# Kernel tuning notes

Hardware: AMD Instinct MI355X
Metric: run time of the kernel (lower is better)

## Reference

```python
import jax, jax.numpy as jnp
import numpy as np

DIM = 2048
NH = 16
NKV = 4
HD = DIM // NH            # 128
KVD = HD * NKV            # 512
MLP = int(DIM * 4.0 * 2 / 3)  # 5461
EPS = 1.1920929e-07       # torch.finfo(float32).eps (nn.RMSNorm default)
ROPE_BASE = 10000.0


def act_quant(x):
    # per-token int8 absmax quantization (BitNet b1.58)
    scale = 127.0 / jnp.clip(jnp.max(jnp.abs(x), axis=-1, keepdims=True), 1e-5)
    return jnp.clip(jnp.round(x * scale), -128.0, 127.0) / scale


def weight_quant(w):
    # ternary weights via mean-absmax scale (BitNet b1.58)
    scale = 1.0 / jnp.clip(jnp.mean(jnp.abs(w)), 1e-5)
    return jnp.clip(jnp.round(w * scale), -1.0, 1.0) / scale


def bitlinear(x, w, b=None):
    # straight-through estimator quantization, then dense matmul
    xq = x + jax.lax.stop_gradient(act_quant(x) - x)
    wq = w + jax.lax.stop_gradient(weight_quant(w) - w)
    y = xq @ wq.T
    return y if b is None else y + b


def rmsnorm(x, w):
    return x * jax.lax.rsqrt(jnp.mean(x * x, axis=-1, keepdims=True) + EPS) * w


def rope_cos_sin(pos, head_dim, dtype):
    inv_freq = 1.0 / (ROPE_BASE ** (jnp.arange(0, head_dim, 2, dtype=jnp.float32) / head_dim))
    freqs = pos[..., None].astype(jnp.float32) * inv_freq  # [B,N,HD/2]
    cos = jnp.repeat(jnp.cos(freqs), 2, axis=-1).astype(dtype)  # interleaved [B,N,HD]
    sin = jnp.repeat(jnp.sin(freqs), 2, axis=-1).astype(dtype)
    return cos, sin


def rotate_interleave(x):
    x1 = x[..., 0::2]
    x2 = x[..., 1::2]
    return jnp.stack([-x2, x1], axis=-1).reshape(x.shape)


def apply_rope(x, cos, sin):
    # x: [B,H,N,HD]; cos/sin: [B,N,HD]
    return x * cos[:, None] + rotate_interleave(x) * sin[:, None]


def setup_inputs() -> dict:
    key = jax.random.key(0)
    ks = jax.random.split(key, 16)
    B, N = 2, 2048
    s = 0.02
    return {
        "x": jax.random.normal(ks[0], (B, N, DIM), jnp.float32),
        "position_ids": jnp.broadcast_to(jnp.arange(N, dtype=jnp.int32), (B, N)),
        "norm1_w": jnp.ones((DIM,), jnp.float32),
        "q_w": jax.random.normal(ks[1], (DIM, DIM), jnp.float32) * s,
        "q_b": jnp.zeros((DIM,), jnp.float32),
        "k_w": jax.random.normal(ks[2], (KVD, DIM), jnp.float32) * s,
        "k_b": jnp.zeros((KVD,), jnp.float32),
        "v_w": jax.random.normal(ks[3], (KVD, DIM), jnp.float32) * s,
        "v_b": jnp.zeros((KVD,), jnp.float32),
        "o_w": jax.random.normal(ks[4], (DIM, DIM), jnp.float32) * s,
        "norm2_w": jnp.ones((DIM,), jnp.float32),
        "gate_w": jax.random.normal(ks[5], (MLP, DIM), jnp.float32) * s,
        "up_w": jax.random.normal(ks[6], (MLP, DIM), jnp.float32) * s,
        "down_w": jax.random.normal(ks[7], (DIM, MLP), jnp.float32) * s,
    }


def reference(x, position_ids, norm1_w, q_w, q_b, k_w, k_b, v_w, v_b, o_w,
              norm2_w, gate_w, up_w, down_w):
    B, N, C = x.shape
    # --- attention ---
    h = rmsnorm(x, norm1_w)
    q = bitlinear(h, q_w, q_b).reshape(B, N, NH, HD).transpose(0, 2, 1, 3)
    k = bitlinear(h, k_w, k_b).reshape(B, N, NKV, HD).transpose(0, 2, 1, 3)
    v = bitlinear(h, v_w, v_b).reshape(B, N, NKV, HD).transpose(0, 2, 1, 3)
    cos, sin = rope_cos_sin(position_ids, HD, x.dtype)
    q = apply_rope(q, cos, sin)
    k = apply_rope(k, cos, sin)
    g = NH // NKV
    k = jnp.repeat(k, g, axis=1)  # GQA head expansion -> [B,NH,N,HD]
    v = jnp.repeat(v, g, axis=1)
    scores = jnp.einsum('bhqd,bhkd->bhqk', q, k) * (HD ** -0.5)
    causal_mask = jnp.triu(jnp.ones((N, N), bool), 1)
    scores = jnp.where(causal_mask, -jnp.inf, scores)
    attn = jax.nn.softmax(scores, axis=-1)
    out = jnp.einsum('bhqk,bhkd->bqhd', attn, v).reshape(B, N, C)
    x = x + bitlinear(out, o_w)
    # --- SwiGLU MLP ---
    h = rmsnorm(x, norm2_w)
    x = x + bitlinear(jax.nn.silu(bitlinear(h, gate_w)) * bitlinear(h, up_w), down_w)
    return x
```

## Files before the change

kernel.cpp:

```cpp
#include <hip/hip_runtime.h>

typedef unsigned short u16;
typedef unsigned int   u32;
typedef unsigned char  u8;

using bf16x8 = __attribute__((ext_vector_type(8))) short;
using f32x4  = __attribute__((ext_vector_type(4))) float;
using i32x4  = __attribute__((ext_vector_type(4))) int;

#define SEQ    2048
#define DIMC   2048
#define TOK    4096
#define QKV_N  3072
#define GU_N   11008
#define MLP_P  5504
#define MLP_R  5461
#define ATT_SCALE 0.08838834764831845f

__device__ __forceinline__ float bf2f(u16 v){ return __uint_as_float(((u32)v) << 16); }
__device__ __forceinline__ u16 f2bf(float f){
  u32 x = __float_as_uint(f);
  u32 r = (x + 0x7fffu + ((x >> 16) & 1u)) >> 16;
  return (u16)r;
}

__device__ __forceinline__ float waveRedSum(float v){
#pragma unroll
  for (int o = 32; o > 0; o >>= 1) v += __shfl_xor(v, o);
  return v;
}
__device__ __forceinline__ float waveRedMax(float v){
#pragma unroll
  for (int o = 32; o > 0; o >>= 1) v = fmaxf(v, __shfl_xor(v, o));
  return v;
}

#define GLD16(gp, lp) __builtin_amdgcn_global_load_lds( \
    (__attribute__((address_space(1))) void*)(gp), \
    (__attribute__((address_space(3))) void*)(lp), 16, 0, 0)

#define FENCE() asm volatile("" ::: "memory")
#define SBAR()  do{ FENCE(); __builtin_amdgcn_s_barrier(); FENCE(); }while(0)
#define VMCNT(n) asm volatile("s_waitcnt vmcnt(" #n ")" ::: "memory")

__global__ __launch_bounds__(256) void k_abssum7(
    const float4* __restrict__ w0, const float4* __restrict__ w1,
    const float4* __restrict__ w2, const float4* __restrict__ w3,
    const float4* __restrict__ w4, const float4* __restrict__ w5,
    const float4* __restrict__ w6, float* __restrict__ sc){
  const int rg = blockIdx.y;
  const float4* w = rg==0?w0: rg==1?w1: rg==2?w2: rg==3?w3: rg==4?w4: rg==5?w5: w6;
  const int n4 = (rg==0||rg==3) ? 1048576 : (rg<4 ? 262144 : 2796032);
  float s = 0.f;
  for (int i = blockIdx.x*256 + threadIdx.x; i < n4; i += gridDim.x*256){
    float4 v = w[i];
    s += fabsf(v.x) + fabsf(v.y) + fabsf(v.z) + fabsf(v.w);
  }
  s = waveRedSum(s);
  __shared__ float sm[4];
  int lane = threadIdx.x & 63, wv = threadIdx.x >> 6;
  if (lane == 0) sm[wv] = s;
  __syncthreads();
  if (threadIdx.x == 0) atomicAdd(sc + rg, sm[0]+sm[1]+sm[2]+sm[3]);
}

__global__ void k_finalize(float* __restrict__ sc){
  if (threadIdx.x == 0){
    const float counts[7] = {4194304.f, 1048576.f, 1048576.f, 4194304.f,
                             11184128.f, 11184128.f, 11184128.f};
    for (int i = 0; i < 7; i++) sc[8+i] = fmaxf(sc[i]/counts[i], 1e-5f);
  }
}

__global__ __launch_bounds__(256) void k_wquant6(
    const float4* __restrict__ w0, const float4* __restrict__ w1,
    const float4* __restrict__ w2, const float4* __restrict__ w3,
    const float4* __restrict__ w4, const float4* __restrict__ w5,
    u32* __restrict__ d0, u32* __restrict__ d1, u32* __restrict__ d2,
    u32* __restrict__ d3, u32* __restrict__ dgu,
    const float* __restrict__ sc){
  const int rg = blockIdx.y;
  const float4* src = rg==0?w0: rg==1?w1: rg==2?w2: rg==3?w3: rg==4?w4: w5;
  const int n4 = (rg==0||rg==3) ? 1048576 : (rg<4 ? 262144 : 2796032);
  float ws = 1.0f / sc[8+rg];
  for (int i = blockIdx.x*256 + threadIdx.x; i < n4; i += gridDim.x*256){
    float4 v = src[i];
    int c0 = (int)fminf(fmaxf(rintf(v.x*ws), -1.f), 1.f);
    int c1 = (int)fminf(fmaxf(rintf(v.y*ws), -1.f), 1.f);
    int c2 = (int)fminf(fmaxf(rintf(v.z*ws), -1.f), 1.f);
    int c3 = (int)fminf(fmaxf(rintf(v.w*ws), -1.f), 1.f);
    u32 pk = (u32)(u8)c0 | ((u32)(u8)c1 << 8) | ((u32)(u8)c2 << 16) | ((u32)(u8)c3 << 24);
    if (rg < 4){
      u32* dst = rg==0?d0: rg==1?d1: rg==2?d2: d3;
      dst[i] = pk;
    } else {
      int row = i >> 9, col = i & 511;
      int rI = 32*(row>>4) + (row&15) + ((rg==5)?16:0);
      dgu[(long)rI*512 + col] = pk;
    }
  }
}

__global__ __launch_bounds__(256) void k_wquant_down(const float* __restrict__ src,
                                                     u32* __restrict__ dst,
                                                     const float* __restrict__ deqp){
  int i = blockIdx.x*256 + threadIdx.x;
  const int total = 2048*(MLP_P/4);
  if (i >= total) return;
  float ws = 1.0f / deqp[0];
  int r = i / (MLP_P/4);
  int c4 = (i - r*(MLP_P/4))*4;
  u32 o = 0;
#pragma unroll
  for (int e = 0; e < 4; e++){
    int c = c4 + e;
    int t = 0;
    if (c < MLP_R) t = (int)fminf(fmaxf(rintf(src[(long)r*MLP_R + c]*ws), -1.f), 1.f);
    o |= (u32)(u8)t << (8*e);
  }
  dst[i] = o;
}

__global__ __launch_bounds__(256) void k_rmsq(const float* __restrict__ in,
                                              const float* __restrict__ nw,
                                              char* __restrict__ outq,
                                              float* __restrict__ rowdeq, int do_norm){
  const int row = blockIdx.x, tid = threadIdx.x;
  const float* xp = in + (long)row * DIMC + tid*8;
  float v[8];
  float4 a0 = *(const float4*)xp;
  float4 a1 = *(const float4*)(xp + 4);
  v[0]=a0.x; v[1]=a0.y; v[2]=a0.z; v[3]=a0.w;
  v[4]=a1.x; v[5]=a1.y; v[6]=a1.z; v[7]=a1.w;
  float ss = 0.f;
#pragma unroll
  for (int j = 0; j < 8; j++) ss += v[j]*v[j];
  __shared__ float sm[8];
  int lane = tid & 63, wv = tid >> 6;
  ss = waveRedSum(ss);
  if (lane == 0) sm[wv] = ss;
  __syncthreads();
  float h[8];
  float amax = 0.f;
  if (do_norm){
    float tot = sm[0]+sm[1]+sm[2]+sm[3];
    float rms = rsqrtf(tot * (1.0f/DIMC) + 1.1920929e-07f);
    float4 w0 = *(const float4*)(nw + tid*8);
    float4 w1 = *(const float4*)(nw + tid*8 + 4);
    float wr8[8] = {w0.x,w0.y,w0.z,w0.w,w1.x,w1.y,w1.z,w1.w};
#pragma unroll
    for (int j = 0; j < 8; j++){ h[j] = v[j]*rms*wr8[j]; amax = fmaxf(amax, fabsf(h[j])); }
  } else {
#pragma unroll
    for (int j = 0; j < 8; j++){ h[j] = v[j]; amax = fmaxf(amax, fabsf(h[j])); }
  }
  amax = waveRedMax(amax);
  if (lane == 0) sm[4+wv] = amax;
  __syncthreads();
  float gmax = fmaxf(fmaxf(sm[4],sm[5]), fmaxf(sm[6],sm[7]));
  float sc = 127.0f / fmaxf(gmax, 1e-5f);
  int2 o;
  char* oc = (char*)&o;
#pragma unroll
  for (int j = 0; j < 8; j++)
    oc[j] = (char)(int)fminf(fmaxf(rintf(h[j]*sc), -128.f), 127.f);
  *(int2*)(outq + (long)row*DIMC + tid*8) = o;
  if (tid == 0) rowdeq[row] = 1.0f / sc;
}

__global__ __launch_bounds__(256) void k_quantb(const u16* __restrict__ in,
                                                char* __restrict__ outq,
                                                float* __restrict__ rowdeq){
  const int row = blockIdx.x, tid = threadIdx.x;
  int4 a = *(const int4*)(in + (long)row*DIMC + tid*8);
  const u16* ap = (const u16*)&a;
  float v[8];
  float amax = 0.f;
#pragma unroll
  for (int j = 0; j < 8; j++){ v[j] = bf2f(ap[j]); amax = fmaxf(amax, fabsf(v[j])); }
  amax = waveRedMax(amax);
  __shared__ float sm[4];
  int lane = tid & 63, wv = tid >> 6;
  if (lane == 0) sm[wv] = amax;
  __syncthreads();
  float gmax = fmaxf(fmaxf(sm[0],sm[1]), fmaxf(sm[2],sm[3]));
  float sc = 127.0f / fmaxf(gmax, 1e-5f);
  int2 o;
  char* oc = (char*)&o;
#pragma unroll
  for (int j = 0; j < 8; j++)
    oc[j] = (char)(int)fminf(fmaxf(rintf(v[j]*sc), -128.f), 127.f);
  *(int2*)(outq + (long)row*DIMC + tid*8) = o;
  if (tid == 0) rowdeq[row] = 1.0f / sc;
}

__global__ __launch_bounds__(256) void k_ropevt2(u16* __restrict__ y,
                                                 const int* __restrict__ pos_ids,
                                                 u16* __restrict__ VT){
  if (blockIdx.x < 4096){
    const int m = blockIdx.x, tid = threadIdx.x;
    __shared__ float cs[64], sn[64];
    if (tid < 64){
      float pos = (float)pos_ids[m];
      float inv = expf((float)tid * -0.14391156831212787f);
      float s, c;
      sincosf(pos * inv, &s, &c);
      cs[tid] = c; sn[tid] = s;
    }
    __syncthreads();
    u32* row = (u32*)(y + (long)m*QKV_N);
#pragma unroll
    for (int it = 0; it < 5; it++){
      int p = it*256 + tid;
      int i = p & 63;
      u32 both = row[p];
      float x0 = bf2f((u16)(both & 0xffffu));
      float x1 = bf2f((u16)(both >> 16));
      float c = cs[i], s = sn[i];
      u16 o0 = f2bf(x0*c - x1*s);
      u16 o1 = f2bf(x1*c + x0*s);
      row[p] = (u32)o0 | ((u32)o1 << 16);
    }
  } else {
    int idx = (int)(blockIdx.x - 4096)*256 + threadIdx.x;
    int d  = idx & 127;
    int hk = (idx >> 7) & 3;
    int b  = (idx >> 9) & 1;
    int tg = idx >> 10;
    int tok0 = tg*8;
    const u16* src = y + ((long)b*SEQ + tok0)*QKV_N + 2560 + hk*128 + d;
    u16 tmp[8];
#pragma unroll
    for (int e = 0; e < 8; e++) tmp[e] = src[(long)e*QKV_N];
    *(int4*)(VT + (((long)(b*4+hk))*128 + d)*SEQ + tok0) = *(int4*)tmp;
  }
}

template<int BM, int BN, int WM, int WN, int MODE>
__global__ __launch_bounds__(512, 2) void k_gemm8(
    const char* __restrict__ A, const char* __restrict__ B,
    int K, int lda, int ldb, int ldc, int ntn,
    const float* __restrict__ rowdeq, const float* __restrict__ deqp,
    const float* __restrict__ bq, const float* __restrict__ bk, const float* __restrict__ bv,
    const float* __restrict__ resid, float* __restrict__ outF, u16* __restrict__ outB)
{
  constexpr int SM = BM/WM, SN = BN/WN;
  constexpr int MR = SM/16, NR = SN/16, MRH = MR/2;
  constexpr int RA = BM/128, RB = BN/128;
  constexpr int ASZ = BM*64, BSZ = BN*64;
  constexpr int BUFSZ = 2*(ASZ+BSZ);
  extern __shared__ __align__(16) char sm8[];

  const int tid = threadIdx.x;
  const int lane = tid & 63, wv = tid >> 6;
  const int wr = wv / WN, wc = wv % WN;
  const int r = lane & 15, qq = lane >> 4;

  const int nwg = gridDim.x;
  const int chunk = nwg >> 3;
  const int lin = blockIdx.x;
  const int swz = (lin & 7)*chunk + (lin >> 3);
  const int mt = swz / ntn, nt = swz - mt*ntn;
  const long m0 = (long)mt*BM, n0 = (long)nt*BN;

  const char* __restrict__ gA = A + m0*lda;
  const char* __restrict__ gB = B + n0*ldb;

  int  soA[RA], soB[RB];
  long goA[RA], goB[RB];
#pragma unroll
  for (int u = 0; u < RA; u++){
    int c = u*512 + tid, row = c >> 2, gp = c & 3, g = gp ^ ((row>>1)&3);
    soA[u] = c*16; goA[u] = (long)row*lda + g*16;
  }
#pragma unroll
  for (int u = 0; u < RB; u++){
    int c = u*512 + tid, row = c >> 2, gp = c & 3, g = gp ^ ((row>>1)&3);
    soB[u] = c*16; goB[u] = (long)row*ldb + g*16;
  }
  const int gsw = (qq ^ ((r>>1)&3))*16;
  const int aoff0 = (wr*SM + r)*64 + gsw;
  const int boff0 = (wc*SN + r)*64 + gsw;

  const int NT = K >> 7;

  i32x4 acc[MR][NR];
#pragma unroll
  for (int i = 0; i < MR; i++)
#pragma unroll
    for (int j = 0; j < NR; j++) acc[i][j] = (i32x4){0,0,0,0};

  auto stA = [&](int tq, int kh){
    char* dst = sm8 + (tq&1)*BUFSZ + kh*ASZ;
    const char* src = gA + (long)tq*128 + kh*64;
#pragma unroll
    for (int u = 0; u < RA; u++) GLD16(src + goA[u], dst + soA[u]);
  };
  auto stB = [&](int tq, int kh){
    char* dst = sm8 + (tq&1)*BUFSZ + 2*ASZ + kh*BSZ;
    const char* src = gB + (long)tq*128 + kh*64;
#pragma unroll
    for (int u = 0; u < RB; u++) GLD16(src + goB[u], dst + soB[u]);
  };

  stA(0,0); stB(0,0); stA(0,1); stB(0,1);
  stA(1,0); stB(1,0);
  if constexpr (RA+RB == 4) VMCNT(4); else VMCNT(3);
  SBAR();

  for (int t = 0; t < NT; t++){
    const char* cA = sm8 + (t&1)*BUFSZ;
    const char* cB = cA + 2*ASZ;
    i32x4 bF[NR];
    {
      i32x4 aF[MRH];
#pragma unroll
      for (int i = 0; i < MRH; i++) aF[i] = *(const i32x4*)(cA + aoff0 + i*1024);
#pragma unroll
      for (int j = 0; j < NR; j++)  bF[j] = *(const i32x4*)(cB + boff0 + j*1024);
      if (t+1 < NT) stA(t+1, 1);
      SBAR();
      __builtin_amdgcn_s_setprio(1);
#pragma unroll
      for (int i = 0; i < MRH; i++)
#pragma unroll
        for (int j = 0; j < NR; j++)
          acc[i][j] = __builtin_amdgcn_mfma_i32_16x16x64_i8(aF[i], bF[j], acc[i][j], 0,0,0);
      __builtin_amdgcn_s_setprio(0);
      SBAR();
    }
    {
      i32x4 aF[MRH];
#pragma unroll
      for (int i = 0; i < MRH; i++) aF[i] = *(const i32x4*)(cA + aoff0 + (MRH+i)*1024);
      if (t+1 < NT) stB(t+1, 1);
      SBAR();
      __builtin_amdgcn_s_setprio(1);
#pragma unroll
      for (int i = 0; i < MRH; i++)
#pragma unroll
        for (int j = 0; j < NR; j++)
          acc[MRH+i][j] = __builtin_amdgcn_mfma_i32_16x16x64_i8(aF[i], bF[j], acc[MRH+i][j], 0,0,0);
      __builtin_amdgcn_s_setprio(0);
      SBAR();
    }
    {
      i32x4 aF[MRH];
#pragma unroll
      for (int i = 0; i < MRH; i++) aF[i] = *(const i32x4*)(cA + ASZ + aoff0 + i*1024);
#pragma unroll
      for (int j = 0; j < NR; j++)  bF[j] = *(const i32x4*)(cB + BSZ + boff0 + j*1024);
      if (t+2 < NT) stA(t+2, 0);
      SBAR();
      __builtin_amdgcn_s_setprio(1);
#pragma unroll
      for (int i = 0; i < MRH; i++)
#pragma unroll
        for (int j = 0; j < NR; j++)
          acc[i][j] = __builtin_amdgcn_mfma_i32_16x16x64_i8(aF[i], bF[j], acc[i][j], 0,0,0);
      __builtin_amdgcn_s_setprio(0);
      SBAR();
    }
    {
      i32x4 aF[MRH];
#pragma unroll
      for (int i = 0; i < MRH; i++) aF[i] = *(const i32x4*)(cA + ASZ + aoff0 + (MRH+i)*1024);
      if (t+2 < NT) stB(t+2, 0);
      SBAR();
      __builtin_amdgcn_s_setprio(1);
#pragma unroll
      for (int i = 0; i < MRH; i++)
#pragma unroll
        for (int j = 0; j < NR; j++)
          acc[MRH+i][j] = __builtin_amdgcn_mfma_i32_16x16x64_i8(aF[i], bF[j], acc[MRH+i][j], 0,0,0);
      __builtin_amdgcn_s_setprio(0);
      if (t + 1 < NT){
        if (t + 2 < NT){ if constexpr (RA+RB == 4) VMCNT(4); else VMCNT(3); }
        else VMCNT(0);
      }
      SBAR();
    }
  }

#pragma unroll
  for (int i = 0; i < MR; i++){
#pragma unroll
    for (int tt = 0; tt < 4; tt++){
      const long row = m0 + wr*SM + 16*i + 4*qq + tt;
      const float rdv = rowdeq[row];
#pragma unroll
      for (int j = 0; j < NR; j++){
        const long col = n0 + wc*SN + 16*j + r;
        float vv = (float)acc[i][j][tt];
        if constexpr (MODE == 0){
          int sec = (col >= 2048) + (col >= 2560);
          float dq = deqp[sec];
          float bias = (sec == 0) ? bq[col] : (sec == 1) ? bk[col-2048] : bv[col-2560];
          outB[row*(long)ldc + col] = f2bf(vv*rdv*dq + bias);
        } else {
          outF[row*(long)ldc + col] = vv*rdv*deqp[0] + resid[row*(long)ldc + col];
        }
      }
    }
  }
}

template<int BM, int MODE>
__global__ __launch_bounds__(256, (BM==128)?3:2) void k_gemm2b(
    const char* __restrict__ A, const char* __restrict__ B,
    int K, int lda, int ldb, int ldc, int vnt, int ntreal,
    const float* __restrict__ rowdeq, const float* __restrict__ deqp,
    const float* __restrict__ resid, float* __restrict__ outF,
    u16* __restrict__ outB)
{
  constexpr int BN = 128;
  constexpr int MR = BM/32, NR = 4, MRH = MR/2;
  constexpr int RA = BM/64, RB = 2;
  constexpr int ASZ = BM*64, BSZ = BN*64;
  constexpr int BUFSZ = ASZ + BSZ;
  __shared__ __align__(16) char sm8[2*BUFSZ];

  const int tid = threadIdx.x;
  const int lane = tid & 63, wv = tid >> 6;
  const int wr = wv >> 1, wc = wv & 1;
  const int r = lane & 15, qq = lane >> 4;

  int mt, nt;
  const int lin = blockIdx.x;
  if constexpr (MODE == 3){
    const int xcd = lin & 7, i0 = lin >> 3;
    const int xcdw = vnt >> 3;
    const int ntl = i0 % xcdw; mt = i0 / xcdw;
    nt = xcd*xcdw + ntl;
    if (nt >= ntreal) return;
  } else {
    const int chunk = gridDim.x >> 3;
    const int swz = (lin & 7)*chunk + (lin >> 3);
    mt = swz / vnt; nt = swz - mt*vnt;
  }
  const long m0 = (long)mt*BM, n0 = (long)nt*BN;

  const char* __restrict__ gA = A + m0*lda;
  const char* __restrict__ gB = B + n0*ldb;

  int  soA[RA], soB[RB];
  long goA[RA], goB[RB];
#pragma unroll
  for (int u = 0; u < RA; u++){
    int c = u*256 + tid, row = c >> 2, g = (c & 3) ^ ((row>>1)&3);
    soA[u] = c*16; goA[u] = (long)row*lda + g*16;
  }
#pragma unroll
  for (int u = 0; u < RB; u++){
    int c = u*256 + tid, row = c >> 2, g = (c & 3) ^ ((row>>1)&3);
    soB[u] = c*16; goB[u] = (long)row*ldb + g*16;
  }
  const int gsw = (qq ^ ((r>>1)&3))*16;
  const int aoff0 = (wr*(BM/2) + r)*64 + gsw;
  const int boff0 = (wc*64 + r)*64 + gsw;

  const int NT = K >> 6;

  i32x4 acc[MR][NR];
#pragma unroll
  for (int i = 0; i < MR; i++)
#pragma unroll
    for (int j = 0; j < NR; j++) acc[i][j] = (i32x4){0,0,0,0};

  auto stA = [&](int tq){
    char* dst = sm8 + (tq&1)*BUFSZ;
    const char* src = gA + (long)tq*64;
#pragma unroll
    for (int u = 0; u < RA; u++) GLD16(src + goA[u], dst + soA[u]);
  };
  auto stB = [&](int tq){
    char* dst = sm8 + (tq&1)*BUFSZ + ASZ;
    const char* src = gB + (long)tq*64;
#pragma unroll
    for (int u = 0; u < RB; u++) GLD16(src + goB[u], dst + soB[u]);
  };

  stA(0); stB(0); stB(1);
  VMCNT(2);
  SBAR();

  for (int t = 0; t < NT; t++){
    const char* cA = sm8 + (t&1)*BUFSZ;
    const char* cB = cA + ASZ;
    i32x4 bF[NR];
    {
      i32x4 aF[MRH];
#pragma unroll
      for (int i = 0; i < MRH; i++) aF[i] = *(const i32x4*)(cA + aoff0 + i*1024);
#pragma unroll
      for (int j = 0; j < NR; j++)  bF[j] = *(const i32x4*)(cB + boff0 + j*1024);
      if (t+1 < NT) stA(t+1);
      SBAR();
      __builtin_amdgcn_s_setprio(1);
#pragma unroll
      for (int i = 0; i < MRH; i++)
#pragma unroll
        for (int j = 0; j < NR; j++)
          acc[i][j] = __builtin_amdgcn_mfma_i32_16x16x64_i8(aF[i], bF[j], acc[i][j], 0,0,0);
      __builtin_amdgcn_s_setprio(0);
      SBAR();
    }
    {
      i32x4 aF[MRH];
#pragma unroll
      for (int i = 0; i < MRH; i++) aF[i] = *(const i32x4*)(cA + aoff0 + (MRH+i)*1024);
      if (t+2 < NT) stB(t+2);
      SBAR();
      __builtin_amdgcn_s_setprio(1);
#pragma unroll
      for (int i = 0; i < MRH; i++)
#pragma unroll
        for (int j = 0; j < NR; j++)
          acc[MRH+i][j] = __builtin_amdgcn_mfma_i32_16x16x64_i8(aF[i], bF[j], acc[MRH+i][j], 0,0,0);
      __builtin_amdgcn_s_setprio(0);
      if (t + 1 < NT){
        if (t + 2 < NT) VMCNT(2); else VMCNT(0);
      }
      SBAR();
    }
  }

#pragma unroll
  for (int i = 0; i < MR; i++){
#pragma unroll
    for (int tt = 0; tt < 4; tt++){
      const long row = m0 + wr*(BM/2) + 16*i + 4*qq + tt;
      const float rdv = rowdeq[row];
      if constexpr (MODE == 3){
        const float dqg = deqp[0], dqu = deqp[1];
#pragma unroll
        for (int j = 0; j < NR; j += 2){
          const long col = n0 + wc*64 + 16*j + r;
          float g = (float)acc[i][j][tt]   * rdv * dqg;
          float u = (float)acc[i][j+1][tt] * rdv * dqu;
          float hv = g * (1.0f/(1.0f + __expf(-g))) * u;
          const long hcol = (col >> 5)*16 + (col & 15);
          outB[row*(long)ldc + hcol] = f2bf(hv);
        }
      } else {
#pragma unroll
        for (int j = 0; j < NR; j++){
          const long col = n0 + wc*64 + 16*j + r;
          float vv = (float)acc[i][j][tt];
          outF[row*(long)ldc + col] = vv*rdv*deqp[0] + resid[row*(long)ldc + col];
        }
      }
    }
  }
}

__global__ __launch_bounds__(256) void k_attn(const u16* __restrict__ Y,
                                              const u16* __restrict__ VT,
                                              u16* __restrict__ O)
{
  __shared__ u16 Ks[64*128];
  __shared__ u16 VTs[128*64];
  __shared__ u16 Ps[64][72];

  const int pp = blockIdx.x;
  const int bh = blockIdx.y;
  const int b = bh >> 4, h = bh & 15, hk = h >> 2;
  const int tid = threadIdx.x;
  const int lane = tid & 63, wv = tid >> 6;
  const int r = lane & 15, qq = lane >> 4;
  const long rowbase = (long)b * SEQ;
  const u16* Kbase = Y + rowbase*QKV_N + 2048 + hk*128;
  const u16* Vbase = VT + ((long)(b*4+hk))*128*SEQ;

  for (int ph = 0; ph < 2; ph++){
    const int qt = ph ? pp : 31 - pp;
    const int q0 = qt * 64;

    bf16x8 qf[4];
#pragma unroll
    for (int kc = 0; kc < 4; kc++)
      qf[kc] = *(const bf16x8*)(Y + (rowbase + q0 + wv*16 + r)*QKV_N + h*128 + kc*32 + qq*8);

#pragma unroll
    for (int rnd = 0; rnd < 4; rnd++){
      int c = rnd*256 + tid;
      int row = c >> 4, g = (c & 15) ^ (row & 7);
      GLD16(Kbase + ((long)(qt*0 + row))*QKV_N + g*8, (char*)Ks + c*16);
    }
#pragma unroll
    for (int rnd = 0; rnd < 4; rnd++){
      int c = rnd*256 + tid;
      int d = c >> 3, g = (c & 7) ^ (d & 7);
      GLD16(Vbase + (long)d*SEQ + g*8, (char*)VTs + c*16);
    }
    __syncthreads();

    f32x4 accO[8];
#pragma unroll
    for (int jn = 0; jn < 8; jn++) accO[jn] = (f32x4){0.f,0.f,0.f,0.f};
    float m_run[4] = {-INFINITY,-INFINITY,-INFINITY,-INFINITY};
    float l_run[4] = {0.f,0.f,0.f,0.f};

    for (int kt = 0; kt <= qt; kt++){
      float sv[4][4];
#pragma unroll
      for (int j = 0; j < 4; j++){
        f32x4 a = (f32x4){0.f,0.f,0.f,0.f};
#pragma unroll
        for (int kc = 0; kc < 4; kc++){
          bf16x8 kf = *(const bf16x8*)(Ks + (16*j + r)*128 + (((kc*4 + qq) ^ (r & 7)))*8);
          a = __builtin_amdgcn_mfma_f32_16x16x32_bf16(qf[kc], kf, a, 0, 0, 0);
        }
#pragma unroll
        for (int t = 0; t < 4; t++) sv[j][t] = a[t] * ATT_SCALE;
      }
      __syncthreads();
      if (kt < qt){
#pragma unroll
        for (int rnd = 0; rnd < 4; rnd++){
          int c = rnd*256 + tid;
          int row = c >> 4, g = (c & 15) ^ (row & 7);
          GLD16(Kbase + ((long)((kt+1)*64 + row))*QKV_N + g*8, (char*)Ks + c*16);
        }
      }
      if (kt == qt){
#pragma unroll
        for (int j = 0; j < 4; j++){
          int key = kt*64 + 16*j + r;
#pragma unroll
          for (int t = 0; t < 4; t++){
            int qr = q0 + wv*16 + 4*qq + t;
            if (key > qr) sv[j][t] = -INFINITY;
          }
        }
      }
#pragma unroll
      for (int t = 0; t < 4; t++){
        float mm = fmaxf(fmaxf(sv[0][t],sv[1][t]), fmaxf(sv[2][t],sv[3][t]));
#pragma unroll
        for (int o = 8; o > 0; o >>= 1) mm = fmaxf(mm, __shfl_xor(mm, o));
        float mnew = fmaxf(m_run[t], mm);
        float alpha = __expf(m_run[t] - mnew);
        m_run[t] = mnew;
        float ps = 0.f;
#pragma unroll
        for (int j = 0; j < 4; j++){
          float p = __expf(sv[j][t] - mnew);
          ps += p;
          Ps[wv*16 + 4*qq + t][16*j + r] = f2bf(p);
        }
#pragma unroll
        for (int o = 8; o > 0; o >>= 1) ps += __shfl_xor(ps, o);
        l_run[t] = l_run[t]*alpha + ps;
#pragma unroll
        for (int jn = 0; jn < 8; jn++) accO[jn][t] *= alpha;
      }
#pragma unroll
      for (int kc = 0; kc < 2; kc++){
        bf16x8 pf = *(const bf16x8*)&Ps[wv*16 + r][kc*32 + qq*8];
#pragma unroll
        for (int jn = 0; jn < 8; jn++){
          bf16x8 vf = *(const bf16x8*)(VTs + (16*jn + r)*64 + (((kc*4 + qq) ^ (r & 7)))*8);
          accO[jn] = __builtin_amdgcn_mfma_f32_16x16x32_bf16(pf, vf, accO[jn], 0, 0, 0);
        }
      }
      __syncthreads();
      if (kt < qt){
#pragma unroll
        for (int rnd = 0; rnd < 4; rnd++){
          int c = rnd*256 + tid;
          int d = c >> 3, g = (c & 7) ^ (d & 7);
          GLD16(Vbase + (long)d*SEQ + (kt+1)*64 + g*8, (char*)VTs + c*16);
        }
      }
    }
    float inv[4];
#pragma unroll
    for (int t = 0; t < 4; t++) inv[t] = 1.0f / l_run[t];
#pragma unroll
    for (int jn = 0; jn < 8; jn++){
#pragma unroll
      for (int t = 0; t < 4; t++){
        long row = rowbase + q0 + wv*16 + 4*qq + t;
        O[row*DIMC + h*128 + 16*jn + r] = f2bf(accO[jn][t]*inv[t]);
      }
    }
    __syncthreads();
  }
}

__global__ __launch_bounds__(256) void k_hquant(const u16* __restrict__ hbuf,
                                                char* __restrict__ qout,
                                                float* __restrict__ rowdeq){
  const int row = blockIdx.x, tid = threadIdx.x;
  const u16* base = hbuf + (long)row * MLP_P;
  float h[24];
  float amax = 0.f;
#pragma unroll
  for (int it = 0; it < 3; it++){
    int chunk = it*256 + tid;
    if (chunk < 688){
      int j0 = chunk*8;
      int4 h4 = *(const int4*)(base + j0);
      const u16* hp = (const u16*)&h4;
#pragma unroll
      for (int e = 0; e < 8; e++){
        float hv = bf2f(hp[e]);
        h[it*8+e] = hv;
        amax = fmaxf(amax, fabsf(hv));
      }
    } else {
#pragma unroll
      for (int e = 0; e < 8; e++) h[it*8+e] = 0.f;
    }
  }
  amax = waveRedMax(amax);
  __shared__ float sm[4];
  int lane = tid & 63, wv = tid >> 6;
  if (lane == 0) sm[wv] = amax;
  __syncthreads();
  float gmax = fmaxf(fmaxf(sm[0],sm[1]), fmaxf(sm[2],sm[3]));
  float sc = 127.0f / fmaxf(gmax, 1e-5f);
#pragma unroll
  for (int it = 0; it < 3; it++){
    int chunk = it*256 + tid;
    if (chunk < 688){
      int j0 = chunk*8;
      int2 o;
      char* oc = (char*)&o;
#pragma unroll
      for (int e = 0; e < 8; e++)
        oc[e] = (char)(int)fminf(fmaxf(rintf(h[it*8+e]*sc), -128.f), 127.f);
      *(int2*)(qout + (long)row*MLP_P + j0) = o;
    }
  }
  if (tid == 0) rowdeq[row] = 1.0f/sc;
}

extern "C" void kernel_launch(void* const* d_in, const int* in_sizes, int n_in,
                              void* d_out, int out_size, void* d_ws, size_t ws_size,
                              hipStream_t stream)
{
  (void)in_sizes; (void)n_in; (void)out_size; (void)ws_size;
  const float* x   = (const float*)d_in[0];
  const int*   pos = (const int*)d_in[1];
  const float* n1w = (const float*)d_in[2];
  const float* qw  = (const float*)d_in[3];
  const float* qb  = (const float*)d_in[4];
  const float* kw  = (const float*)d_in[5];
  const float* kb  = (const float*)d_in[6];
  const float* vw  = (const float*)d_in[7];
  const float* vb  = (const float*)d_in[8];
  const float* ow  = (const float*)d_in[9];
  const float* n2w = (const float*)d_in[10];
  const float* gw  = (const float*)d_in[11];
  const float* uw  = (const float*)d_in[12];
  const float* dw  = (const float*)d_in[13];
  float* out = (float*)d_out;
  char* ws = (char*)d_ws;

  static int attr_done = 0;
  if (!attr_done){
    hipFuncSetAttribute(reinterpret_cast<const void*>(k_gemm8<256,128,4,2,0>),
                        hipFuncAttributeMaxDynamicSharedMemorySize, 98304);
    attr_done = 1;
  }

  float* sc   = (float*)ws;
  char* Wqkv  = ws + 256;
  char* Wo    = ws + 6291712;
  char* Wgu   = ws + 10486016;
  char* Wd    = ws + 33030400;
  char* actq  = ws + 44302592;
  char* swq   = ws + 52691200;
  float* rd   = (float*)(ws + 75235584);
  char* xreg  = ws + 75252224;
  u16* yqkv   = (u16*)xreg;
  u16* attnb  = (u16*)(xreg + 25165824);
  u16* vT     = (u16*)(xreg + 58720256);
  u16* hbuf   = (u16*)xreg;

  hipMemsetAsync(sc, 0, 64, stream);
  hipMemsetAsync(Wgu, 0, 11008l*2048, stream);
  k_abssum7<<<dim3(512,7),256,0,stream>>>((const float4*)qw, (const float4*)kw,
                                          (const float4*)vw, (const float4*)ow,
                                          (const float4*)gw, (const float4*)uw,
                                          (const float4*)dw, sc);
  k_finalize<<<1,64,0,stream>>>(sc);
  k_wquant6<<<dim3(512,6),256,0,stream>>>((const float4*)qw, (const float4*)kw,
                                          (const float4*)vw, (const float4*)ow,
                                          (const float4*)gw, (const float4*)uw,
                                          (u32*)Wqkv, (u32*)(Wqkv + 2048l*2048),
                                          (u32*)(Wqkv + 2560l*2048), (u32*)Wo,
                                          (u32*)Wgu, sc);
  k_wquant_down<<<11008,256,0,stream>>>(dw, (u32*)Wd, sc+14);

  k_rmsq<<<4096,256,0,stream>>>(x, n1w, actq, rd, 1);
  k_gemm8<256,128,4,2,0><<<384,512,98304,stream>>>(actq, Wqkv, 2048, 2048, 2048, 3072, 24,
                                          rd, sc+8, qb, kb, vb, nullptr, nullptr, yqkv);
  k_ropevt2<<<5120,256,0,stream>>>(yqkv, pos, vT);
  k_attn<<<dim3(16,32),256,0,stream>>>(yqkv, vT, attnb);
  k_quantb<<<4096,256,0,stream>>>(attnb, actq, rd);
  k_gemm2b<128,1><<<512,256,0,stream>>>(actq, Wo, 2048, 2048, 2048, 2048, 16, 16,
                                        rd, sc+11, x, out, nullptr);

  k_rmsq<<<4096,256,0,stream>>>(out, n2w, actq, rd, 1);
  k_gemm2b<256,3><<<1408,256,0,stream>>>(actq, Wgu, 2048, 2048, 2048, MLP_P, 88, 86,
                                         rd, sc+12, nullptr, nullptr, hbuf);
  k_hquant<<<4096,256,0,stream>>>(hbuf, swq, rd);
  k_gemm2b<128,1><<<512,256,0,stream>>>(swq, Wd, 5504, 5504, 5504, 2048, 16, 16,
                                        rd, sc+14, out, out, nullptr);
}
```

Baseline: 673.5 us.

## Drop finalize kernel and memset, reuse gemm2b for QKV projection

The separate k_finalize launch is removed, and each consumer now computes the mean-abs weight scale inline from the raw sums. The 22 MB memset of the gate/up weight buffer is replaced by having k_wquant6 write zeros for padded rows itself. The dedicated 512-thread k_gemm8 QKV kernel is deleted in favour of a new MODE 0 epilogue in k_gemm2b with 128-row tiles. This cuts launches and memory traffic, but the QKV GEMM now uses a smaller-tile kernel whose efficiency may differ.

```diff
diff --git a/kernel.cpp b/kernel.cpp
--- a/kernel.cpp
+++ b/kernel.cpp
@@ -42,6 +42,10 @@
 #define FENCE() asm volatile("" ::: "memory")
 #define SBAR()  do{ FENCE(); __builtin_amdgcn_s_barrier(); FENCE(); }while(0)
 #define VMCNT(n) asm volatile("s_waitcnt vmcnt(" #n ")" ::: "memory")
+
+__device__ __forceinline__ float deq_of(float sum, float cnt){
+  return fmaxf(sum/cnt, 1e-5f);
+}
 
 __global__ __launch_bounds__(256) void k_abssum7(
     const float4* __restrict__ w0, const float4* __restrict__ w1,
@@ -64,14 +68,6 @@
   if (threadIdx.x == 0) atomicAdd(sc + rg, sm[0]+sm[1]+sm[2]+sm[3]);
 }
 
-__global__ void k_finalize(float* __restrict__ sc){
-  if (threadIdx.x == 0){
-    const float counts[7] = {4194304.f, 1048576.f, 1048576.f, 4194304.f,
-                             11184128.f, 11184128.f, 11184128.f};
-    for (int i = 0; i < 7; i++) sc[8+i] = fmaxf(sc[i]/counts[i], 1e-5f);
-  }
-}
-
 __global__ __launch_bounds__(256) void k_wquant6(
     const float4* __restrict__ w0, const float4* __restrict__ w1,
     const float4* __restrict__ w2, const float4* __restrict__ w3,
@@ -81,20 +77,25 @@
     const float* __restrict__ sc){
   const int rg = blockIdx.y;
   const float4* src = rg==0?w0: rg==1?w1: rg==2?w2: rg==3?w3: rg==4?w4: w5;
-  const int n4 = (rg==0||rg==3) ? 1048576 : (rg<4 ? 262144 : 2796032);
-  float ws = 1.0f / sc[8+rg];
+  const int n4 = (rg==0||rg==3) ? 1048576 : (rg<4 ? 262144 : 2818048);
+  const float cnt = (rg==0||rg==3) ? 4194304.f : (rg<4 ? 1048576.f : 11184128.f);
+  float ws = 1.0f / deq_of(sc[rg], cnt);
   for (int i = blockIdx.x*256 + threadIdx.x; i < n4; i += gridDim.x*256){
-    float4 v = src[i];
-    int c0 = (int)fminf(fmaxf(rintf(v.x*ws), -1.f), 1.f);
-    int c1 = (int)fminf(fmaxf(rintf(v.y*ws), -1.f), 1.f);
-    int c2 = (int)fminf(fmaxf(rintf(v.z*ws), -1.f), 1.f);
-    int c3 = (int)fminf(fmaxf(rintf(v.w*ws), -1.f), 1.f);
-    u32 pk = (u32)(u8)c0 | ((u32)(u8)c1 << 8) | ((u32)(u8)c2 << 16) | ((u32)(u8)c3 << 24);
+    u32 pk = 0;
+    int row = i >> 9;
+    if (rg < 4 || row < MLP_R){
+      float4 v = src[i];
+      int c0 = (int)fminf(fmaxf(rintf(v.x*ws), -1.f), 1.f);
+      int c1 = (int)fminf(fmaxf(rintf(v.y*ws), -1.f), 1.f);
+      int c2 = (int)fminf(fmaxf(rintf(v.z*ws), -1.f), 1.f);
+      int c3 = (int)fminf(fmaxf(rintf(v.w*ws), -1.f), 1.f);
+      pk = (u32)(u8)c0 | ((u32)(u8)c1 << 8) | ((u32)(u8)c2 << 16) | ((u32)(u8)c3 << 24);
+    }
     if (rg < 4){
       u32* dst = rg==0?d0: rg==1?d1: rg==2?d2: d3;
       dst[i] = pk;
     } else {
-      int row = i >> 9, col = i & 511;
+      int col = i & 511;
       int rI = 32*(row>>4) + (row&15) + ((rg==5)?16:0);
       dgu[(long)rI*512 + col] = pk;
     }
@@ -103,11 +104,11 @@
 
 __global__ __launch_bounds__(256) void k_wquant_down(const float* __restrict__ src,
                                                      u32* __restrict__ dst,
-                                                     const float* __restrict__ deqp){
+                                                     const float* __restrict__ sc6){
   int i = blockIdx.x*256 + threadIdx.x;
   const int total = 2048*(MLP_P/4);
   if (i >= total) return;
-  float ws = 1.0f / deqp[0];
+  float ws = 1.0f / deq_of(sc6[0], 11184128.f);
   int r = i / (MLP_P/4);
   int c4 = (i - r*(MLP_P/4))*4;
   u32 o = 0;
@@ -236,180 +237,12 @@
   }
 }
 
-template<int BM, int BN, int WM, int WN, int MODE>
-__global__ __launch_bounds__(512, 2) void k_gemm8(
-    const char* __restrict__ A, const char* __restrict__ B,
-    int K, int lda, int ldb, int ldc, int ntn,
-    const float* __restrict__ rowdeq, const float* __restrict__ deqp,
-    const float* __restrict__ bq, const float* __restrict__ bk, const float* __restrict__ bv,
-    const float* __restrict__ resid, float* __restrict__ outF, u16* __restrict__ outB)
-{
-  constexpr int SM = BM/WM, SN = BN/WN;
-  constexpr int MR = SM/16, NR = SN/16, MRH = MR/2;
-  constexpr int RA = BM/128, RB = BN/128;
-  constexpr int ASZ = BM*64, BSZ = BN*64;
-  constexpr int BUFSZ = 2*(ASZ+BSZ);
-  extern __shared__ __align__(16) char sm8[];
-
-  const int tid = threadIdx.x;
-  const int lane = tid & 63, wv = tid >> 6;
-  const int wr = wv / WN, wc = wv % WN;
-  const int r = lane & 15, qq = lane >> 4;
-
-  const int nwg = gridDim.x;
-  const int chunk = nwg >> 3;
-  const int lin = blockIdx.x;
-  const int swz = (lin & 7)*chunk + (lin >> 3);
-  const int mt = swz / ntn, nt = swz - mt*ntn;
-  const long m0 = (long)mt*BM, n0 = (long)nt*BN;
-
-  const char* __restrict__ gA = A + m0*lda;
-  const char* __restrict__ gB = B + n0*ldb;
-
-  int  soA[RA], soB[RB];
-  long goA[RA], goB[RB];
-#pragma unroll
-  for (int u = 0; u < RA; u++){
-    int c = u*512 + tid, row = c >> 2, gp = c & 3, g = gp ^ ((row>>1)&3);
-    soA[u] = c*16; goA[u] = (long)row*lda + g*16;
-  }
-#pragma unroll
-  for (int u = 0; u < RB; u++){
-    int c = u*512 + tid, row = c >> 2, gp = c & 3, g = gp ^ ((row>>1)&3);
-    soB[u] = c*16; goB[u] = (long)row*ldb + g*16;
-  }
-  const int gsw = (qq ^ ((r>>1)&3))*16;
-  const int aoff0 = (wr*SM + r)*64 + gsw;
-  const int boff0 = (wc*SN + r)*64 + gsw;
-
-  const int NT = K >> 7;
-
-  i32x4 acc[MR][NR];
-#pragma unroll
-  for (int i = 0; i < MR; i++)
-#pragma unroll
-    for (int j = 0; j < NR; j++) acc[i][j] = (i32x4){0,0,0,0};
-
-  auto stA = [&](int tq, int kh){
-    char* dst = sm8 + (tq&1)*BUFSZ + kh*ASZ;
-    const char* src = gA + (long)tq*128 + kh*64;
-#pragma unroll
-    for (int u = 0; u < RA; u++) GLD16(src + goA[u], dst + soA[u]);
-  };
-  auto stB = [&](int tq, int kh){
-    char* dst = sm8 + (tq&1)*BUFSZ + 2*ASZ + kh*BSZ;
-    const char* src = gB + (long)tq*128 + kh*64;
-#pragma unroll
-    for (int u = 0; u < RB; u++) GLD16(src + goB[u], dst + soB[u]);
-  };
-
-  stA(0,0); stB(0,0); stA(0,1); stB(0,1);
-  stA(1,0); stB(1,0);
-  if constexpr (RA+RB == 4) VMCNT(4); else VMCNT(3);
-  SBAR();
-
-  for (int t = 0; t < NT; t++){
-    const char* cA = sm8 + (t&1)*BUFSZ;
-    const char* cB = cA + 2*ASZ;
-    i32x4 bF[NR];
-    {
-      i32x4 aF[MRH];
-#pragma unroll
-      for (int i = 0; i < MRH; i++) aF[i] = *(const i32x4*)(cA + aoff0 + i*1024);
-#pragma unroll
-      for (int j = 0; j < NR; j++)  bF[j] = *(const i32x4*)(cB + boff0 + j*1024);
-      if (t+1 < NT) stA(t+1, 1);
-      SBAR();
-      __builtin_amdgcn_s_setprio(1);
-#pragma unroll
-      for (int i = 0; i < MRH; i++)
-#pragma unroll
-        for (int j = 0; j < NR; j++)
-          acc[i][j] = __builtin_amdgcn_mfma_i32_16x16x64_i8(aF[i], bF[j], acc[i][j], 0,0,0);
-      __builtin_amdgcn_s_setprio(0);
-      SBAR();
-    }
-    {
-      i32x4 aF[MRH];
-#pragma unroll
-      for (int i = 0; i < MRH; i++) aF[i] = *(const i32x4*)(cA + aoff0 + (MRH+i)*1024);
-      if (t+1 < NT) stB(t+1, 1);
-      SBAR();
-      __builtin_amdgcn_s_setprio(1);
-#pragma unroll
-      for (int i = 0; i < MRH; i++)
-#pragma unroll
-        for (int j = 0; j < NR; j++)
-          acc[MRH+i][j] = __builtin_amdgcn_mfma_i32_16x16x64_i8(aF[i], bF[j], acc[MRH+i][j], 0,0,0);
-      __builtin_amdgcn_s_setprio(0);
-      SBAR();
-    }
-    {
-      i32x4 aF[MRH];
-#pragma unroll
-      for (int i = 0; i < MRH; i++) aF[i] = *(const i32x4*)(cA + ASZ + aoff0 + i*1024);
-#pragma unroll
-      for (int j = 0; j < NR; j++)  bF[j] = *(const i32x4*)(cB + BSZ + boff0 + j*1024);
-      if (t+2 < NT) stA(t+2, 0);
-      SBAR();
-      __builtin_amdgcn_s_setprio(1);
-#pragma unroll
-      for (int i = 0; i < MRH; i++)
-#pragma unroll
-        for (int j = 0; j < NR; j++)
-          acc[i][j] = __builtin_amdgcn_mfma_i32_16x16x64_i8(aF[i], bF[j], acc[i][j], 0,0,0);
-      __builtin_amdgcn_s_setprio(0);
-      SBAR();
-    }
-    {
-      i32x4 aF[MRH];
-#pragma unroll
-      for (int i = 0; i < MRH; i++) aF[i] = *(const i32x4*)(cA + ASZ + aoff0 + (MRH+i)*1024);
-      if (t+2 < NT) stB(t+2, 0);
-      SBAR();
-      __builtin_amdgcn_s_setprio(1);
-#pragma unroll
-      for (int i = 0; i < MRH; i++)
-#pragma unroll
-        for (int j = 0; j < NR; j++)
-          acc[MRH+i][j] = __builtin_amdgcn_mfma_i32_16x16x64_i8(aF[i], bF[j], acc[MRH+i][j], 0,0,0);
-      __builtin_amdgcn_s_setprio(0);
-      if (t + 1 < NT){
-        if (t + 2 < NT){ if constexpr (RA+RB == 4) VMCNT(4); else VMCNT(3); }
-        else VMCNT(0);
-      }
-      SBAR();
-    }
-  }
-
-#pragma unroll
-  for (int i = 0; i < MR; i++){
-#pragma unroll
-    for (int tt = 0; tt < 4; tt++){
-      const long row = m0 + wr*SM + 16*i + 4*qq + tt;
-      const float rdv = rowdeq[row];
-#pragma unroll
-      for (int j = 0; j < NR; j++){
-        const long col = n0 + wc*SN + 16*j + r;
-        float vv = (float)acc[i][j][tt];
-        if constexpr (MODE == 0){
-          int sec = (col >= 2048) + (col >= 2560);
-          float dq = deqp[sec];
-          float bias = (sec == 0) ? bq[col] : (sec == 1) ? bk[col-2048] : bv[col-2560];
-          outB[row*(long)ldc + col] = f2bf(vv*rdv*dq + bias);
-        } else {
-          outF[row*(long)ldc + col] = vv*rdv*deqp[0] + resid[row*(long)ldc + col];
-        }
-      }
-    }
-  }
-}
-
 template<int BM, int MODE>
 __global__ __launch_bounds__(256, (BM==128)?3:2) void k_gemm2b(
     const char* __restrict__ A, const char* __restrict__ B,
     int K, int lda, int ldb, int ldc, int vnt, int ntreal,
-    const float* __restrict__ rowdeq, const float* __restrict__ deqp,
+    const float* __restrict__ rowdeq, const float* __restrict__ sums, float cnt,
+    const float* __restrict__ bq, const float* __restrict__ bk, const float* __restrict__ bv,
     const float* __restrict__ resid, float* __restrict__ outF,
     u16* __restrict__ outB)
 {
@@ -531,8 +364,20 @@
     for (int tt = 0; tt < 4; tt++){
       const long row = m0 + wr*(BM/2) + 16*i + 4*qq + tt;
       const float rdv = rowdeq[row];
-      if constexpr (MODE == 3){
-        const float dqg = deqp[0], dqu = deqp[1];
+      if constexpr (MODE == 0){
+#pragma unroll
+        for (int j = 0; j < NR; j++){
+          const long col = n0 + wc*64 + 16*j + r;
+          int sec = (col >= 2048) + (col >= 2560);
+          float cn = (sec == 0) ? 4194304.f : 1048576.f;
+          float dq = deq_of(sums[sec], cn);
+          float bias = (sec == 0) ? bq[col] : (sec == 1) ? bk[col-2048] : bv[col-2560];
+          float vv = (float)acc[i][j][tt];
+          outB[row*(long)ldc + col] = f2bf(vv*rdv*dq + bias);
+        }
+      } else if constexpr (MODE == 3){
+        const float dqg = deq_of(sums[0], 11184128.f);
+        const float dqu = deq_of(sums[1], 11184128.f);
 #pragma unroll
         for (int j = 0; j < NR; j += 2){
           const long col = n0 + wc*64 + 16*j + r;
@@ -543,11 +388,12 @@
           outB[row*(long)ldc + hcol] = f2bf(hv);
         }
       } else {
+        const float deq = deq_of(sums[0], cnt);
 #pragma unroll
         for (int j = 0; j < NR; j++){
           const long col = n0 + wc*64 + 16*j + r;
           float vv = (float)acc[i][j][tt];
-          outF[row*(long)ldc + col] = vv*rdv*deqp[0] + resid[row*(long)ldc + col];
+          outF[row*(long)ldc + col] = vv*rdv*deq + resid[row*(long)ldc + col];
         }
       }
     }
@@ -759,13 +605,6 @@
   float* out = (float*)d_out;
   char* ws = (char*)d_ws;
 
-  static int attr_done = 0;
-  if (!attr_done){
-    hipFuncSetAttribute(reinterpret_cast<const void*>(k_gemm8<256,128,4,2,0>),
-                        hipFuncAttributeMaxDynamicSharedMemorySize, 98304);
-    attr_done = 1;
-  }
-
   float* sc   = (float*)ws;
   char* Wqkv  = ws + 256;
   char* Wo    = ws + 6291712;
@@ -781,33 +620,34 @@
   u16* hbuf   = (u16*)xreg;
 
   hipMemsetAsync(sc, 0, 64, stream);
-  hipMemsetAsync(Wgu, 0, 11008l*2048, stream);
   k_abssum7<<<dim3(512,7),256,0,stream>>>((const float4*)qw, (const float4*)kw,
                                           (const float4*)vw, (const float4*)ow,
                                           (const float4*)gw, (const float4*)uw,
                                           (const float4*)dw, sc);
-  k_finalize<<<1,64,0,stream>>>(sc);
   k_wquant6<<<dim3(512,6),256,0,stream>>>((const float4*)qw, (const float4*)kw,
                                           (const float4*)vw, (const float4*)ow,
                                           (const float4*)gw, (const float4*)uw,
                                           (u32*)Wqkv, (u32*)(Wqkv + 2048l*2048),
                                           (u32*)(Wqkv + 2560l*2048), (u32*)Wo,
                                           (u32*)Wgu, sc);
-  k_wquant_down<<<11008,256,0,stream>>>(dw, (u32*)Wd, sc+14);
+  k_wquant_down<<<11008,256,0,stream>>>(dw, (u32*)Wd, sc+6);
 
   k_rmsq<<<4096,256,0,stream>>>(x, n1w, actq, rd, 1);
-  k_gemm8<256,128,4,2,0><<<384,512,98304,stream>>>(actq, Wqkv, 2048, 2048, 2048, 3072, 24,
-                                          rd, sc+8, qb, kb, vb, nullptr, nullptr, yqkv);
+  k_gemm2b<128,0><<<768,256,0,stream>>>(actq, Wqkv, 2048, 2048, 2048, 3072, 24, 24,
+                                        rd, sc, 0.f, qb, kb, vb, nullptr, nullptr, yqkv);
   k_ropevt2<<<5120,256,0,stream>>>(yqkv, pos, vT);
   k_attn<<<dim3(16,32),256,0,stream>>>(yqkv, vT, attnb);
   k_quantb<<<4096,256,0,stream>>>(attnb, actq, rd);
   k_gemm2b<128,1><<<512,256,0,stream>>>(actq, Wo, 2048, 2048, 2048, 2048, 16, 16,
-                                        rd, sc+11, x, out, nullptr);
+                                        rd, sc+3, 4194304.f, nullptr, nullptr, nullptr,
+                                        x, out, nullptr);
 
   k_rmsq<<<4096,256,0,stream>>>(out, n2w, actq, rd, 1);
   k_gemm2b<256,3><<<1408,256,0,stream>>>(actq, Wgu, 2048, 2048, 2048, MLP_P, 88, 86,
-                                         rd, sc+12, nullptr, nullptr, hbuf);
+                                         rd, sc+4, 0.f, nullptr, nullptr, nullptr,
+                                         nullptr, nullptr, hbuf);
   k_hquant<<<4096,256,0,stream>>>(hbuf, swq, rd);
   k_gemm2b<128,1><<<512,256,0,stream>>>(swq, Wd, 5504, 5504, 5504, 2048, 16, 16,
-                                        rd, sc+14, out, out, nullptr);
-}
+                                        rd, sc+6, 11184128.f, nullptr, nullptr, nullptr,
+                                        out, out, nullptr);
+}
```

Result: faster. 654.6 us (-2.8%).
